# Performance work log

Hardware: AMD Instinct MI355X
Metric: run time of the kernel (lower is better)

Reference implementation:

```python
import jax, jax.numpy as jnp
import numpy as np

EPS = 1e-5  # instance-norm epsilon (NormalizeLayer over spatial axes)

def instance_norm(x):
    # normalize over spatial axes (1,2) per sample, per channel
    mean = jnp.mean(x, axis=(1, 2), keepdims=True)
    var = jnp.var(x, axis=(1, 2), keepdims=True)
    return (x - mean) / jnp.sqrt(var + EPS)

def l2norm(x, axis=-1):
    return x / jnp.sqrt(jnp.sum(x * x, axis=axis, keepdims=True) + 1e-12)

def setup_inputs() -> dict:
    key = jax.random.key(0)
    ks = jax.random.split(key, 5)
    B, H, W, C = 4, 64, 64, 256
    content = jax.random.normal(ks[0], (B, H, W, C), jnp.float32)
    style = jax.random.normal(ks[1], (B, H, W, C), jnp.float32)
    scale = 1.0 / np.sqrt(C)
    Wq = jax.random.normal(ks[2], (C, C), jnp.float32) * scale
    Wk = jax.random.normal(ks[3], (C, C), jnp.float32) * scale
    Wv = jax.random.normal(ks[4], (C, C), jnp.float32) * scale
    bq = jnp.zeros((C,), jnp.float32)
    bk = jnp.zeros((C,), jnp.float32)
    bv = jnp.zeros((C,), jnp.float32)
    return {"content": content, "style": style, "Wq": Wq, "bq": bq,
            "Wk": Wk, "bk": bk, "Wv": Wv, "bv": bv}

def reference(content, style, Wq, bq, Wk, bk, Wv, bv):
    B, H, W, C = content.shape
    N = H * W
    norm_content = instance_norm(content)
    norm_style = instance_norm(style)
    # 1x1 convs == per-pixel linear layers
    Q = (jnp.einsum('bhwc,cd->bhwd', norm_content, Wq) + bq).reshape(B, N, C)
    K = (jnp.einsum('bhwc,cd->bhwd', norm_style, Wk) + bk).reshape(B, N, C)
    V = (jnp.einsum('bhwc,cd->bhwd', style, Wv) + bv).reshape(B, N, C)
    # cosine-similarity attention (Dot with normalize=True)
    attn = jnp.einsum('bnc,bmc->bnm', l2norm(Q), l2norm(K))  # [B, N, N]
    A = jax.nn.softmax(attn, axis=-1)
    M = jnp.einsum('bnm,bmc->bnc', A, V)                 # weighted mean
    S2 = jnp.einsum('bnm,bmc->bnc', A, V * V) - M * M    # weighted variance
    S2 = jax.nn.relu(S2)
    # safe sqrt: grad-safe at exactly 0 (matches sqrt(relu(x)) values)
    S = jnp.where(S2 > 0, jnp.sqrt(jnp.where(S2 > 0, S2, 1.0)), 0.0)
    S = S.reshape(B, H, W, C)
    M = M.reshape(B, H, W, C)
    return S * norm_content + M
```

## Files before the change

kernel.cpp:

```cpp
#include <hip/hip_runtime.h>
#include <cstdint>

#define BB 4
#define NN 4096
#define CC 256

typedef __attribute__((ext_vector_type(8))) short bf16x8;
typedef __attribute__((ext_vector_type(4))) short bf16x4;
typedef __attribute__((ext_vector_type(4))) float f32x4;
typedef unsigned int u32;
typedef __attribute__((ext_vector_type(4))) u32 u32x4;

#define MFMA_FP8(a, b, c)  __builtin_amdgcn_mfma_f32_16x16x32_fp8_fp8((a), (b), (c), 0, 0, 0)

#define WAITCNT(vm, xp, lgkm) (((vm) & 0xF) | (((vm) >> 4) << 14) | ((xp) << 4) | ((lgkm) << 8))

__device__ __forceinline__ unsigned short f2bf(float f) {
  union { float f; unsigned u; } v; v.f = f;
  unsigned r = v.u + 0x7fffu + ((v.u >> 16) & 1u);
  return (unsigned short)(r >> 16);
}
__device__ __forceinline__ u32 pk4_fp8(float a, float b, float c, float d) {
  u32 v = (u32)__builtin_amdgcn_cvt_pk_fp8_f32(a, b, 0, false);
  v = (u32)__builtin_amdgcn_cvt_pk_fp8_f32(c, d, (int)v, true);
  return v;
}
__device__ __forceinline__ unsigned char fp8_1(float a) {
  return (unsigned char)(((u32)__builtin_amdgcn_cvt_pk_fp8_f32(a, a, 0, false)) & 0xff);
}

typedef __attribute__((address_space(3))) unsigned int lds_u32;
typedef __attribute__((address_space(1))) unsigned int glb_u32;

__device__ __forceinline__ void async_cp16(const void* g, void* l) {
  __builtin_amdgcn_global_load_lds((const glb_u32*)g,
                                   (lds_u32*)(unsigned)(unsigned long long)l,
                                   16, 0, 0);
}

__global__ __launch_bounds__(256) void transpose_w(const float* __restrict__ Wq,
                                                   const float* __restrict__ Wk,
                                                   const float* __restrict__ Wv,
                                                   unsigned char* __restrict__ Wt8) {
  __shared__ float sT[64 * 65];
  int blk = blockIdx.x;
  int z = blk / 16, tl = blk % 16;
  int c0 = (tl >> 2) * 64, d0 = (tl & 3) * 64;
  const float* W = (z == 0) ? Wq : ((z == 1) ? Wk : Wv);
  #pragma unroll
  for (int i = 0; i < 16; ++i) {
    int e = i * 256 + threadIdx.x;
    int c = e >> 6, d = e & 63;
    sT[c * 65 + d] = W[(size_t)(c0 + c) * CC + d0 + d];
  }
  __syncthreads();
  #pragma unroll
  for (int i = 0; i < 16; ++i) {
    int e = i * 256 + threadIdx.x;
    int d = e >> 6, c = e & 63;
    Wt8[(size_t)z * 65536 + (size_t)(d0 + d) * CC + c0 + c] = fp8_1(sT[c * 65 + d]);
  }
}

__global__ __launch_bounds__(256) void stats_partial(const float* __restrict__ content,
                                                     const float* __restrict__ style,
                                                     float* __restrict__ sums) {
  int blk = blockIdx.x;
  int t = blk >> 9, b = (blk >> 7) & 3, chunk = blk & 127;
  const float* X = t ? style : content;
  int c = threadIdx.x;
  const float* base = X + ((size_t)b * NN + (size_t)chunk * 32) * CC + c;
  float s = 0.f, ss = 0.f;
  #pragma unroll 8
  for (int r = 0; r < 32; ++r) {
    float x = base[(size_t)r * CC];
    s += x; ss += x * x;
  }
  atomicAdd(&sums[((t * 2 + 0) * BB + b) * CC + c], s);
  atomicAdd(&sums[((t * 2 + 1) * BB + b) * CC + c], ss);
}

__global__ __launch_bounds__(256) void stats_finalize(const float* __restrict__ sums,
                                                      float* __restrict__ stats) {
  int i = blockIdx.x * 256 + threadIdx.x;
  int t = i >> 10, bc = i & 1023;
  float s = sums[(t * 2 + 0) * 1024 + bc];
  float ss = sums[(t * 2 + 1) * 1024 + bc];
  float m = s * (1.0f / NN);
  float var = ss * (1.0f / NN) - m * m;
  stats[(t * 2 + 0) * 1024 + bc] = m;
  stats[(t * 2 + 1) * 1024 + bc] = rsqrtf(var + 1e-5f);
}

__global__ __launch_bounds__(256, 2) void qkv_kernel(
    const float* __restrict__ content, const float* __restrict__ style,
    const unsigned char* __restrict__ Wt8,
    const float* __restrict__ bq, const float* __restrict__ bk, const float* __restrict__ bv,
    const float* __restrict__ stats,
    unsigned char* __restrict__ Qn, unsigned char* __restrict__ Kn,
    unsigned char* __restrict__ Vct) {
  __shared__ __align__(16) char sW[32768];
  __shared__ __align__(16) char sX[32768];

  int tid = threadIdx.x;
  int wid = tid >> 6, lane = tid & 63, quad = lane >> 4, l16 = lane & 15;
  int uwid = __builtin_amdgcn_readfirstlane(wid);
  int tileid = blockIdx.x;
  int z = blockIdx.y;
  int gr0 = tileid * 128;
  int b = gr0 >> 12;

  const float* X = (z == 0) ? content : style;
  int statt = (z == 0) ? 0 : 1;
  const float* mean = stats + ((statt * 2 + 0) * BB + b) * CC;
  const float* rstd = stats + ((statt * 2 + 1) * BB + b) * CC;
  bool donorm = (z < 2);

  #pragma unroll
  for (int i = 0; i < 8; ++i) {
    int lin = i * 256 + tid;
    int row = lin >> 4, c16 = lin & 15;
    int c = c16 * 16;
    const float* xr = X + (size_t)(gr0 + row) * CC + c;
    f32x4 x0 = *(const f32x4*)(xr + 0);
    f32x4 x1 = *(const f32x4*)(xr + 4);
    f32x4 x2 = *(const f32x4*)(xr + 8);
    f32x4 x3 = *(const f32x4*)(xr + 12);
    if (donorm) {
      f32x4 m0 = *(const f32x4*)(mean + c + 0), r0 = *(const f32x4*)(rstd + c + 0);
      f32x4 m1 = *(const f32x4*)(mean + c + 4), r1 = *(const f32x4*)(rstd + c + 4);
      f32x4 m2 = *(const f32x4*)(mean + c + 8), r2 = *(const f32x4*)(rstd + c + 8);
      f32x4 m3 = *(const f32x4*)(mean + c + 12), r3 = *(const f32x4*)(rstd + c + 12);
      x0 = (x0 - m0) * r0; x1 = (x1 - m1) * r1;
      x2 = (x2 - m2) * r2; x3 = (x3 - m3) * r3;
    }
    u32x4 pk;
    pk.x = pk4_fp8(x0.x, x0.y, x0.z, x0.w);
    pk.y = pk4_fp8(x1.x, x1.y, x1.z, x1.w);
    pk.z = pk4_fp8(x2.x, x2.y, x2.z, x2.w);
    pk.w = pk4_fp8(x3.x, x3.y, x3.z, x3.w);
    *(u32x4*)(sX + row * 256 + ((c16 ^ (row & 15)) * 16)) = pk;
  }

  f32x4 zero4 = {0.f, 0.f, 0.f, 0.f};
  f32x4 acc[2][16];
  #pragma unroll
  for (int i = 0; i < 2; ++i)
    #pragma unroll
    for (int j = 0; j < 16; ++j) acc[i][j] = zero4;

  const unsigned char* wb = Wt8 + (size_t)z * 65536;

  for (int half = 0; half < 2; ++half) {
    __syncthreads();
    #pragma unroll
    for (int it = 0; it < 8; ++it) {
      int L = it * 256 + wid * 64 + lane;
      int d = L >> 3;
      int c16 = (L & 7) ^ (d & 7);
      async_cp16(wb + (size_t)d * 256 + half * 128 + c16 * 16,
                 sW + (size_t)(it * 256 + uwid * 64) * 16);
    }
    __syncthreads();

    long a[2][4];
    #pragma unroll
    for (int mf = 0; mf < 2; ++mf) {
      int row = wid * 32 + mf * 16 + l16;
      #pragma unroll
      for (int kc = 0; kc < 4; ++kc) {
        int chunk = half * 8 + kc * 2 + (quad >> 1);
        a[mf][kc] = *(const long*)(sX + row * 256 + ((chunk ^ (row & 15)) * 16) + (quad & 1) * 8);
      }
    }
    #pragma unroll
    for (int nf = 0; nf < 16; ++nf) {
      int d = nf * 16 + l16;
      #pragma unroll
      for (int kc = 0; kc < 4; ++kc) {
        long bw = *(const long*)(sW + d * 128 + (((kc * 2 + (quad >> 1)) ^ (d & 7)) * 16) + (quad & 1) * 8);
        acc[0][nf] = MFMA_FP8(a[0][kc], bw, acc[0][nf]);
        acc[1][nf] = MFMA_FP8(a[1][kc], bw, acc[1][nf]);
      }
    }
  }

  const float* bias = (z == 0) ? bq : ((z == 1) ? bk : bv);
  #pragma unroll
  for (int nf = 0; nf < 16; ++nf) {
    float bb_ = bias[nf * 16 + l16];
    #pragma unroll
    for (int mf = 0; mf < 2; ++mf) {
      acc[mf][nf].x += bb_; acc[mf][nf].y += bb_;
      acc[mf][nf].z += bb_; acc[mf][nf].w += bb_;
    }
  }

  if (z < 2) {
    unsigned char* O = (z == 0) ? Qn : Kn;
    #pragma unroll
    for (int mf = 0; mf < 2; ++mf) {
      f32x4 ss = zero4;
      #pragma unroll
      for (int nf = 0; nf < 16; ++nf) ss += acc[mf][nf] * acc[mf][nf];
      #pragma unroll
      for (int m = 1; m < 16; m <<= 1) {
        ss.x += __shfl_xor(ss.x, m, 64);
        ss.y += __shfl_xor(ss.y, m, 64);
        ss.z += __shfl_xor(ss.z, m, 64);
        ss.w += __shfl_xor(ss.w, m, 64);
      }
      f32x4 rq;
      rq.x = rsqrtf(ss.x + 1e-12f); rq.y = rsqrtf(ss.y + 1e-12f);
      rq.z = rsqrtf(ss.z + 1e-12f); rq.w = rsqrtf(ss.w + 1e-12f);
      int r0 = wid * 32 + mf * 16 + quad * 4;
      #pragma unroll
      for (int nf = 0; nf < 16; ++nf) {
        int col = nf * 16 + l16;
        u32 p01 = (u32)__builtin_amdgcn_cvt_pk_fp8_f32(acc[mf][nf].x * rq.x, acc[mf][nf].y * rq.y, 0, false);
        u32 p23 = (u32)__builtin_amdgcn_cvt_pk_fp8_f32(acc[mf][nf].z * rq.z, acc[mf][nf].w * rq.w, 0, false);
        O[(size_t)(gr0 + r0 + 0) * CC + col] = (unsigned char)(p01 & 0xff);
        O[(size_t)(gr0 + r0 + 1) * CC + col] = (unsigned char)((p01 >> 8) & 0xff);
        O[(size_t)(gr0 + r0 + 2) * CC + col] = (unsigned char)(p23 & 0xff);
        O[(size_t)(gr0 + r0 + 3) * CC + col] = (unsigned char)((p23 >> 8) & 0xff);
      }
    }
  } else {
    char* sOT = sX;
    int n_in_b = gr0 & (NN - 1);
    __syncthreads();
    #pragma unroll
    for (int pass = 0; pass < 2; ++pass) {
      #pragma unroll
      for (int mf = 0; mf < 2; ++mf) {
        int j = wid * 2 + mf;
        #pragma unroll
        for (int nf = 0; nf < 16; ++nf) {
          int col = nf * 16 + l16;
          f32x4 v = acc[mf][nf];
          f32x4 w = pass ? (v * v) : v;
          u32 pk = pk4_fp8(w.x, w.y, w.z, w.w);
          *(u32*)(sOT + col * 128 + ((j ^ (col & 7)) * 16) + quad * 4) = pk;
        }
      }
      __syncthreads();
      unsigned char* orow = Vct + ((size_t)(b * 512 + (pass ? 256 : 0) + tid)) * NN + n_in_b;
      #pragma unroll
      for (int j = 0; j < 8; ++j) {
        u32x4 val = *(const u32x4*)(sOT + tid * 128 + ((j ^ (tid & 7)) * 16));
        *(u32x4*)(orow + j * 16) = val;
      }
      __syncthreads();
    }
  }
}

__global__ __launch_bounds__(512, 2) void flash_kernel(
    const unsigned char* __restrict__ Qn,
    const unsigned char* __restrict__ Kn,
    const unsigned char* __restrict__ Vct,
    const float* __restrict__ content,
    const float* __restrict__ stats,
    float* __restrict__ out) {
  __shared__ __align__(16) char smem[32768 + 65536 + 8192 + 256];
  char* sKb = smem;
  char* sVb = smem + 32768;
  char* sPb = smem + 98304;
  float* sL = (float*)(smem + 106496);
  float* sE2 = (float*)smem;

  int tid = threadIdx.x;
  int wid = tid >> 6, lane = tid & 63, quad = lane >> 4, l16 = lane & 15;
  int uwid = __builtin_amdgcn_readfirstlane(wid);

  int id = blockIdx.x;
  int b = (id >> 1) & 3;
  int tile = ((id >> 3) << 1) | (id & 1);
  int q0 = tile * 64;

  int qh = (wid & 1) * 32;
  int kb0 = (wid >> 1) * 16;
  int cw = wid * 64;

  long qf[2][8];
  #pragma unroll
  for (int ng = 0; ng < 2; ++ng) {
    int row = q0 + qh + ng * 16 + l16;
    const unsigned char* base = Qn + (((size_t)b * NN + row) << 8);
    #pragma unroll
    for (int kf = 0; kf < 8; ++kf)
      qf[ng][kf] = *(const long*)(base + kf * 32 + quad * 8);
  }
  __builtin_amdgcn_s_waitcnt(WAITCNT(0, 7, 15));

  if (tid < 64) sL[tid] = 0.f;

  const unsigned char* kbp = Kn + (((size_t)b * NN) << 8);
  const unsigned char* vbp = Vct + ((size_t)b * 512) * NN;

  auto stageK = [&](int k0, int buf) {
    char* dst = sKb + buf * 16384;
    #pragma unroll
    for (int it = 0; it < 2; ++it) {
      int L = it * 512 + wid * 64 + lane;
      int ky = L >> 4, s = L & 15;
      int c16 = s ^ (ky & 15);
      async_cp16(kbp + (((size_t)(k0 + ky)) << 8) + c16 * 16,
                 dst + (size_t)(it * 512 + uwid * 64) * 16);
    }
  };
  auto stageV = [&](int k0, int buf) {
    char* dst = sVb + buf * 32768;
    #pragma unroll
    for (int it = 0; it < 4; ++it) {
      int L = it * 512 + wid * 64 + lane;
      int r128 = L >> 3, s8 = L & 7;
      int x = s8 ^ (r128 & 7);
      int ch = (r128 << 1) | (x >> 2);
      int k16 = x & 3;
      async_cp16(vbp + (size_t)ch * NN + k0 + k16 * 16,
                 dst + (size_t)(it * 512 + uwid * 64) * 16);
    }
  };

  f32x4 zero4 = {0.f, 0.f, 0.f, 0.f};
  f32x4 om[4][4];
  #pragma unroll
  for (int i = 0; i < 4; ++i)
    #pragma unroll
    for (int j = 0; j < 4; ++j) om[i][j] = zero4;
  float Lr[2] = {0.f, 0.f};
  long vf[2][4];

  int krow = kb0 + l16;
  int krowoff = krow * 256;
  int khalf = (quad & 1) * 8;

  auto s_phase = [&](int kt) {
    const char* sKc = sKb + (kt & 1) * 16384;
    char* sPc = sPb + (kt & 1) * 4096;
    f32x4 t0 = zero4, t1 = zero4;
    #pragma unroll
    for (int kf = 0; kf < 8; ++kf) {
      int slot = (kf * 2 + (quad >> 1)) ^ (krow & 15);
      long ak = *(const long*)(sKc + krowoff + slot * 16 + khalf);
      t0 = MFMA_FP8(ak, qf[0][kf], t0);
      t1 = MFMA_FP8(ak, qf[1][kf], t1);
    }
    #pragma unroll
    for (int ng = 0; ng < 2; ++ng) {
      f32x4 sv = ng ? t1 : t0;
      float p0 = __expf(sv.x), p1 = __expf(sv.y), p2 = __expf(sv.z), p3 = __expf(sv.w);
      Lr[ng] += p0 + p1 + p2 + p3;
      u32 w = pk4_fp8(p0, p1, p2, p3);
      int q = qh + ng * 16 + l16;
      int c = (kb0 >> 2) + quad;
      *(u32*)(sPc + q * 64 + ((c ^ (q & 14)) * 4)) = w;
    }
    const char* sVc = sVb + (kt & 1) * 32768;
    #pragma unroll
    for (int ks = 0; ks < 2; ++ks) {
      int c16 = ks * 2 + (quad >> 1);
      #pragma unroll
      for (int nf = 0; nf < 4; ++nf) {
        int ch = cw + nf * 16 + l16;
        vf[ks][nf] = *(const long*)(sVc + (ch >> 1) * 128 +
                        (((ch & 1) * 4 + c16) ^ ((ch >> 1) & 7)) * 16 + khalf);
      }
    }
  };

  stageK(0, 0);  stageV(0, 0);
  stageK(64, 1); stageV(64, 1);
  __builtin_amdgcn_s_waitcnt(WAITCNT(6, 7, 15));
  __builtin_amdgcn_s_barrier();
  s_phase(0);
  __builtin_amdgcn_s_waitcnt(WAITCNT(63, 7, 0));
  __builtin_amdgcn_s_barrier();

  for (int kt = 0; kt < 64; ++kt) {
    int nk = ((kt + 2) & 63) * 64;
    stageK(nk, kt & 1);
    stageV(nk, kt & 1);

    const char* sPc = sPb + (kt & 1) * 4096;
    long pf[2][4];
    #pragma unroll
    for (int ks = 0; ks < 2; ++ks)
      #pragma unroll
      for (int mf = 0; mf < 4; ++mf) {
        int q = mf * 16 + l16;
        int c = ks * 8 + quad * 2;
        pf[ks][mf] = *(const long*)(sPc + q * 64 + ((c ^ (q & 14)) * 4));
      }

    #pragma unroll
    for (int ks = 0; ks < 2; ++ks)
      #pragma unroll
      for (int nf = 0; nf < 4; ++nf)
        #pragma unroll
        for (int mf = 0; mf < 4; ++mf)
          om[mf][nf] = MFMA_FP8(pf[ks][mf], vf[ks][nf], om[mf][nf]);

    __builtin_amdgcn_s_waitcnt(WAITCNT(6, 7, 15));
    if (kt < 63) s_phase(kt + 1);

    __builtin_amdgcn_s_waitcnt(WAITCNT(63, 7, 0));
    __builtin_amdgcn_s_barrier();
  }

  #pragma unroll
  for (int ng = 0; ng < 2; ++ng) {
    Lr[ng] += __shfl_xor(Lr[ng], 16, 64);
    Lr[ng] += __shfl_xor(Lr[ng], 32, 64);
  }
  if (quad == 0) {
    atomicAdd(&sL[qh + 0 + l16], Lr[0]);
    atomicAdd(&sL[qh + 16 + l16], Lr[1]);
  }
  __builtin_amdgcn_s_waitcnt(WAITCNT(0, 7, 0));
  __builtin_amdgcn_s_barrier();

  if (wid >= 4) {
    #pragma unroll
    for (int mf = 0; mf < 4; ++mf) {
      #pragma unroll
      for (int nf = 0; nf < 4; ++nf) {
        int ch = (wid - 4) * 64 + nf * 16 + l16;
        int cidx = (mf * 4 + quad) ^ (ch & 15);
        *(f32x4*)(sE2 + ch * 64 + cidx * 4) = om[mf][nf];
      }
    }
  }
  __syncthreads();

  if (wid < 4) {
    const float* meanc = stats + (0 * BB + b) * CC;
    const float* rstdc = stats + (1 * BB + b) * CC;
    float linv[4][4];
    #pragma unroll
    for (int mf = 0; mf < 4; ++mf)
      #pragma unroll
      for (int r = 0; r < 4; ++r)
        linv[mf][r] = 1.0f / sL[mf * 16 + quad * 4 + r];
    #pragma unroll
    for (int nf = 0; nf < 4; ++nf) {
      int ch = cw + nf * 16 + l16;
      float mc = meanc[ch], rc = rstdc[ch];
      #pragma unroll
      for (int mf = 0; mf < 4; ++mf) {
        int cidx = (mf * 4 + quad) ^ (ch & 15);
        f32x4 vv = *(const f32x4*)(sE2 + ch * 64 + cidx * 4);
        f32x4 ov = om[mf][nf];
        #pragma unroll
        for (int r = 0; r < 4; ++r) {
          int row = mf * 16 + quad * 4 + r;
          float li = linv[mf][r];
          float ovr = (r == 0) ? ov.x : (r == 1) ? ov.y : (r == 2) ? ov.z : ov.w;
          float vvr = (r == 0) ? vv.x : (r == 1) ? vv.y : (r == 2) ? vv.z : vv.w;
          float M = ovr * li;
          float E2 = vvr * li;
          float S2 = E2 - M * M;
          float S = (S2 > 0.f) ? sqrtf(S2) : 0.f;
          size_t gi = (((size_t)b * NN + q0 + row) << 8) + ch;
          float xh = (content[gi] - mc) * rc;
          out[gi] = S * xh + M;
        }
      }
    }
  }
}

extern "C" void kernel_launch(void* const* d_in, const int* in_sizes, int n_in,
                              void* d_out, int out_size, void* d_ws, size_t ws_size,
                              hipStream_t stream) {
  const float* content = (const float*)d_in[0];
  const float* style   = (const float*)d_in[1];
  const float* Wq = (const float*)d_in[2];
  const float* bq = (const float*)d_in[3];
  const float* Wk = (const float*)d_in[4];
  const float* bk = (const float*)d_in[5];
  const float* Wv = (const float*)d_in[6];
  const float* bv = (const float*)d_in[7];
  char* ws = (char*)d_ws;

  float* sums        = (float*)(ws + 0);
  float* stats       = (float*)(ws + 16384);
  unsigned char* Wt8 = (unsigned char*)(ws + 32768);
  unsigned char* Qn  = (unsigned char*)(ws + 229376);
  unsigned char* Kn  = (unsigned char*)(ws + 4423680);
  unsigned char* Vct = (unsigned char*)(ws + 8617984);
  float* outp = (float*)d_out;

  hipMemsetAsync(d_ws, 0, 16384, stream);
  hipLaunchKernelGGL(transpose_w, dim3(48), dim3(256), 0, stream, Wq, Wk, Wv, Wt8);
  hipLaunchKernelGGL(stats_partial, dim3(1024), dim3(256), 0, stream, content, style, sums);
  hipLaunchKernelGGL(stats_finalize, dim3(8), dim3(256), 0, stream, sums, stats);
  hipLaunchKernelGGL(qkv_kernel, dim3(128, 3), dim3(256), 0, stream,
                     content, style, Wt8, bq, bk, bv, stats, Qn, Kn, Vct);
  hipLaunchKernelGGL(flash_kernel, dim3(256), dim3(512), 0, stream,
                     Qn, Kn, Vct, content, stats, outp);
}
```

Measured before the change: 208.0 us.

## Halve flash query tile to 32 rows, single-buffer V, double occupancy

The attention kernel now processes 32 query rows per block instead of 64 and launches twice as many blocks. V staging drops from double to single buffering, and the S-phase splits the MFMA chain into two independent accumulators. Shared memory and register use per block shrink, so launch bounds allow 4 blocks per CU instead of 2, which targets better latency hiding. The cost is that each K/V tile is loaded from L2 twice as often per query, and V loads are less overlapped because there is only one buffer.

```diff
diff --git a/kernel.cpp b/kernel.cpp
--- a/kernel.cpp
+++ b/kernel.cpp
@@ -255,18 +255,18 @@
   }
 }
 
-__global__ __launch_bounds__(512, 2) void flash_kernel(
+__global__ __launch_bounds__(512, 4) void flash_kernel(
     const unsigned char* __restrict__ Qn,
     const unsigned char* __restrict__ Kn,
     const unsigned char* __restrict__ Vct,
     const float* __restrict__ content,
     const float* __restrict__ stats,
     float* __restrict__ out) {
-  __shared__ __align__(16) char smem[32768 + 65536 + 8192 + 256];
+  __shared__ __align__(16) char smem[32768 + 32768 + 4096 + 128];
   char* sKb = smem;
-  char* sVb = smem + 32768;
-  char* sPb = smem + 98304;
-  float* sL = (float*)(smem + 106496);
+  char* sV  = smem + 32768;
+  char* sPb = smem + 65536;
+  float* sL = (float*)(smem + 69632);
   float* sE2 = (float*)smem;
 
   int tid = threadIdx.x;
@@ -276,24 +276,23 @@
   int id = blockIdx.x;
   int b = (id >> 1) & 3;
   int tile = ((id >> 3) << 1) | (id & 1);
-  int q0 = tile * 64;
-
-  int qh = (wid & 1) * 32;
-  int kb0 = (wid >> 1) * 16;
+  int q0 = tile * 32;
+
+  int qh = (wid >> 2) * 16;
+  int kb0 = (wid & 3) * 16;
   int cw = wid * 64;
 
-  long qf[2][8];
-  #pragma unroll
-  for (int ng = 0; ng < 2; ++ng) {
-    int row = q0 + qh + ng * 16 + l16;
+  long qf[8];
+  {
+    int row = q0 + qh + l16;
     const unsigned char* base = Qn + (((size_t)b * NN + row) << 8);
     #pragma unroll
     for (int kf = 0; kf < 8; ++kf)
-      qf[ng][kf] = *(const long*)(base + kf * 32 + quad * 8);
+      qf[kf] = *(const long*)(base + kf * 32 + quad * 8);
   }
   __builtin_amdgcn_s_waitcnt(WAITCNT(0, 7, 15));
 
-  if (tid < 64) sL[tid] = 0.f;
+  if (tid < 32) sL[tid] = 0.f;
 
   const unsigned char* kbp = Kn + (((size_t)b * NN) << 8);
   const unsigned char* vbp = Vct + ((size_t)b * 512) * NN;
@@ -309,8 +308,7 @@
                  dst + (size_t)(it * 512 + uwid * 64) * 16);
     }
   };
-  auto stageV = [&](int k0, int buf) {
-    char* dst = sVb + buf * 32768;
+  auto stageV = [&](int k0) {
     #pragma unroll
     for (int it = 0; it < 4; ++it) {
       int L = it * 512 + wid * 64 + lane;
@@ -319,17 +317,17 @@
       int ch = (r128 << 1) | (x >> 2);
       int k16 = x & 3;
       async_cp16(vbp + (size_t)ch * NN + k0 + k16 * 16,
-                 dst + (size_t)(it * 512 + uwid * 64) * 16);
+                 sV + (size_t)(it * 512 + uwid * 64) * 16);
     }
   };
 
   f32x4 zero4 = {0.f, 0.f, 0.f, 0.f};
-  f32x4 om[4][4];
-  #pragma unroll
-  for (int i = 0; i < 4; ++i)
+  f32x4 om[2][4];
+  #pragma unroll
+  for (int i = 0; i < 2; ++i)
     #pragma unroll
     for (int j = 0; j < 4; ++j) om[i][j] = zero4;
-  float Lr[2] = {0.f, 0.f};
+  float Lr = 0.f;
   long vf[2][4];
 
   int krow = kb0 + l16;
@@ -338,57 +336,53 @@
 
   auto s_phase = [&](int kt) {
     const char* sKc = sKb + (kt & 1) * 16384;
-    char* sPc = sPb + (kt & 1) * 4096;
-    f32x4 t0 = zero4, t1 = zero4;
-    #pragma unroll
-    for (int kf = 0; kf < 8; ++kf) {
-      int slot = (kf * 2 + (quad >> 1)) ^ (krow & 15);
-      long ak = *(const long*)(sKc + krowoff + slot * 16 + khalf);
-      t0 = MFMA_FP8(ak, qf[0][kf], t0);
-      t1 = MFMA_FP8(ak, qf[1][kf], t1);
-    }
-    #pragma unroll
-    for (int ng = 0; ng < 2; ++ng) {
-      f32x4 sv = ng ? t1 : t0;
-      float p0 = __expf(sv.x), p1 = __expf(sv.y), p2 = __expf(sv.z), p3 = __expf(sv.w);
-      Lr[ng] += p0 + p1 + p2 + p3;
-      u32 w = pk4_fp8(p0, p1, p2, p3);
-      int q = qh + ng * 16 + l16;
-      int c = (kb0 >> 2) + quad;
-      *(u32*)(sPc + q * 64 + ((c ^ (q & 14)) * 4)) = w;
-    }
-    const char* sVc = sVb + (kt & 1) * 32768;
+    char* sPc = sPb + (kt & 1) * 2048;
+    f32x4 ta = zero4, tb = zero4;
+    #pragma unroll
+    for (int kf = 0; kf < 8; kf += 2) {
+      int sa = (kf * 2 + (quad >> 1)) ^ (krow & 15);
+      long aka = *(const long*)(sKc + krowoff + sa * 16 + khalf);
+      ta = MFMA_FP8(aka, qf[kf], ta);
+      int sb = ((kf + 1) * 2 + (quad >> 1)) ^ (krow & 15);
+      long akb = *(const long*)(sKc + krowoff + sb * 16 + khalf);
+      tb = MFMA_FP8(akb, qf[kf + 1], tb);
+    }
+    f32x4 sv = ta + tb;
+    float p0 = __expf(sv.x), p1 = __expf(sv.y), p2 = __expf(sv.z), p3 = __expf(sv.w);
+    Lr += p0 + p1 + p2 + p3;
+    u32 w = pk4_fp8(p0, p1, p2, p3);
+    int q = qh + l16;
+    int c = (kb0 >> 2) + quad;
+    *(u32*)(sPc + q * 64 + ((c ^ (q & 14)) * 4)) = w;
     #pragma unroll
     for (int ks = 0; ks < 2; ++ks) {
       int c16 = ks * 2 + (quad >> 1);
       #pragma unroll
       for (int nf = 0; nf < 4; ++nf) {
         int ch = cw + nf * 16 + l16;
-        vf[ks][nf] = *(const long*)(sVc + (ch >> 1) * 128 +
+        vf[ks][nf] = *(const long*)(sV + (ch >> 1) * 128 +
                         (((ch & 1) * 4 + c16) ^ ((ch >> 1) & 7)) * 16 + khalf);
       }
     }
   };
 
-  stageK(0, 0);  stageV(0, 0);
-  stageK(64, 1); stageV(64, 1);
-  __builtin_amdgcn_s_waitcnt(WAITCNT(6, 7, 15));
+  stageK(0, 0);  stageV(0);  stageK(64, 1);
+  __builtin_amdgcn_s_waitcnt(WAITCNT(2, 7, 15));
   __builtin_amdgcn_s_barrier();
   s_phase(0);
   __builtin_amdgcn_s_waitcnt(WAITCNT(63, 7, 0));
   __builtin_amdgcn_s_barrier();
 
   for (int kt = 0; kt < 64; ++kt) {
-    int nk = ((kt + 2) & 63) * 64;
-    stageK(nk, kt & 1);
-    stageV(nk, kt & 1);
-
-    const char* sPc = sPb + (kt & 1) * 4096;
-    long pf[2][4];
+    stageV(((kt + 1) & 63) * 64);
+    stageK(((kt + 2) & 63) * 64, kt & 1);
+
+    const char* sPc = sPb + (kt & 1) * 2048;
+    long pf[2][2];
     #pragma unroll
     for (int ks = 0; ks < 2; ++ks)
       #pragma unroll
-      for (int mf = 0; mf < 4; ++mf) {
+      for (int mf = 0; mf < 2; ++mf) {
         int q = mf * 16 + l16;
         int c = ks * 8 + quad * 2;
         pf[ks][mf] = *(const long*)(sPc + q * 64 + ((c ^ (q & 14)) * 4));
@@ -399,36 +393,30 @@
       #pragma unroll
       for (int nf = 0; nf < 4; ++nf)
         #pragma unroll
-        for (int mf = 0; mf < 4; ++mf)
+        for (int mf = 0; mf < 2; ++mf)
           om[mf][nf] = MFMA_FP8(pf[ks][mf], vf[ks][nf], om[mf][nf]);
 
-    __builtin_amdgcn_s_waitcnt(WAITCNT(6, 7, 15));
+    __builtin_amdgcn_s_waitcnt(WAITCNT(2, 7, 15));
     if (kt < 63) s_phase(kt + 1);
 
     __builtin_amdgcn_s_waitcnt(WAITCNT(63, 7, 0));
     __builtin_amdgcn_s_barrier();
   }
 
-  #pragma unroll
-  for (int ng = 0; ng < 2; ++ng) {
-    Lr[ng] += __shfl_xor(Lr[ng], 16, 64);
-    Lr[ng] += __shfl_xor(Lr[ng], 32, 64);
-  }
-  if (quad == 0) {
-    atomicAdd(&sL[qh + 0 + l16], Lr[0]);
-    atomicAdd(&sL[qh + 16 + l16], Lr[1]);
-  }
+  Lr += __shfl_xor(Lr, 16, 64);
+  Lr += __shfl_xor(Lr, 32, 64);
+  if (quad == 0) atomicAdd(&sL[qh + l16], Lr);
   __builtin_amdgcn_s_waitcnt(WAITCNT(0, 7, 0));
   __builtin_amdgcn_s_barrier();
 
   if (wid >= 4) {
     #pragma unroll
-    for (int mf = 0; mf < 4; ++mf) {
+    for (int mf = 0; mf < 2; ++mf) {
       #pragma unroll
       for (int nf = 0; nf < 4; ++nf) {
         int ch = (wid - 4) * 64 + nf * 16 + l16;
-        int cidx = (mf * 4 + quad) ^ (ch & 15);
-        *(f32x4*)(sE2 + ch * 64 + cidx * 4) = om[mf][nf];
+        int cidx = (mf * 4 + quad) ^ (ch & 7);
+        *(f32x4*)(sE2 + ch * 32 + cidx * 4) = om[mf][nf];
       }
     }
   }
@@ -437,9 +425,9 @@
   if (wid < 4) {
     const float* meanc = stats + (0 * BB + b) * CC;
     const float* rstdc = stats + (1 * BB + b) * CC;
-    float linv[4][4];
-    #pragma unroll
-    for (int mf = 0; mf < 4; ++mf)
+    float linv[2][4];
+    #pragma unroll
+    for (int mf = 0; mf < 2; ++mf)
       #pragma unroll
       for (int r = 0; r < 4; ++r)
         linv[mf][r] = 1.0f / sL[mf * 16 + quad * 4 + r];
@@ -448,9 +436,9 @@
       int ch = cw + nf * 16 + l16;
       float mc = meanc[ch], rc = rstdc[ch];
       #pragma unroll
-      for (int mf = 0; mf < 4; ++mf) {
-        int cidx = (mf * 4 + quad) ^ (ch & 15);
-        f32x4 vv = *(const f32x4*)(sE2 + ch * 64 + cidx * 4);
+      for (int mf = 0; mf < 2; ++mf) {
+        int cidx = (mf * 4 + quad) ^ (ch & 7);
+        f32x4 vv = *(const f32x4*)(sE2 + ch * 32 + cidx * 4);
         f32x4 ov = om[mf][nf];
         #pragma unroll
         for (int r = 0; r < 4; ++r) {
@@ -498,6 +486,6 @@
   hipLaunchKernelGGL(stats_finalize, dim3(8), dim3(256), 0, stream, sums, stats);
   hipLaunchKernelGGL(qkv_kernel, dim3(128, 3), dim3(256), 0, stream,
                      content, style, Wt8, bq, bk, bv, stats, Qn, Kn, Vct);
-  hipLaunchKernelGGL(flash_kernel, dim3(256), dim3(512), 0, stream,
+  hipLaunchKernelGGL(flash_kernel, dim3(512), dim3(512), 0, stream,
                      Qn, Kn, Vct, content, stats, outp);
 }
```

Result: slower. 225.6 us (+8.5%).
